# Performance work log

Measured on AMD Instinct MI355X. Metric: run time of the kernel, lower is better.

Reference implementation:

```python
import jax, jax.numpy as jnp
import numpy as np

PATCH = 15  # patch_size (odd, per extract_patches arithmetic)


def _extract_patches(vol, centroids, P):
    """vol: (B,C,H,W,D) float; centroids: (B,N,3) int (x->H, y->W, z->D).
    Returns (B,N,C,P,P,P) with the valid region placed at the patch origin and
    zero padding at the high end of each axis (matches F.pad end-padding)."""
    B, C, H, Wd, D = vol.shape
    half = P // 2
    c = centroids.astype(jnp.int32)                      # (B,N,3)
    dims = jnp.array([H, Wd, D], dtype=jnp.int32)
    starts = jnp.maximum(c - half, 0)                    # (B,N,3)
    ends = jnp.minimum(c + half + 1, dims)               # (B,N,3)
    r = jnp.arange(P, dtype=jnp.int32)
    idx = starts[..., None] + r                          # (B,N,3,P)
    mask = idx < ends[..., None]                         # (B,N,3,P)
    idxc = jnp.minimum(idx, (dims - 1)[None, None, :, None])  # clamp for safe gather

    def one(vol_b, ix, iy, iz, m):
        # vol_b (C,H,W,D); ix/iy/iz (N,P); m (N,3,P)
        p = vol_b[:, ix[:, :, None, None], iy[:, None, :, None], iz[:, None, None, :]]
        p = jnp.transpose(p, (1, 0, 2, 3, 4))            # (N,C,P,P,P)
        m3 = (m[:, 0][:, :, None, None]
              & m[:, 1][:, None, :, None]
              & m[:, 2][:, None, None, :])               # (N,P,P,P)
        return jnp.where(m3[:, None], p, jnp.zeros((), vol_b.dtype))

    return jax.vmap(one)(vol, idxc[:, :, 0], idxc[:, :, 1], idxc[:, :, 2], mask)


def setup_inputs() -> dict:
    key = jax.random.key(0)
    k1, k2, k3 = jax.random.split(key, 3)
    B, C, H, W_, D = 2, 32, 96, 96, 96
    N, F = 64, 1024
    P = PATCH
    x = jax.random.normal(k1, (B, C, H, W_, D), dtype=jnp.float32)
    centroids = jax.random.randint(k2, (B, N, 3), 0, 96, dtype=jnp.int32)
    W = jax.random.normal(k3, (C * P ** 3, F), dtype=jnp.float32) * 0.01
    b = jnp.zeros((F,), dtype=jnp.float32)
    return {"x": x, "centroids": centroids, "W": W, "b": b}


def reference(x, centroids, W, b):
    P = PATCH
    patches = _extract_patches(x, centroids, P)          # (B,N,C,P,P,P)
    B, N = patches.shape[:2]
    flat = patches.reshape(B * N, -1)                    # (B*N, C*P^3)
    out = flat @ W + b                                   # feature_extraction_model
    return out.reshape(B, N, -1)
```

## Files before the change

### kernel.cpp

```cpp
#include <hip/hip_runtime.h>

typedef __attribute__((ext_vector_type(8))) __bf16 bf16x8;
typedef __attribute__((ext_vector_type(8))) unsigned short ushort8;
typedef __attribute__((ext_vector_type(4))) float f32x4;

constexpr int C_ = 32, NN = 64;
constexpr int PK = 3375;
constexpr int K_TOT = 108000;
constexpr int F_TOT = 1024;
constexpr int M_TOT = 128;
constexpr int KSTEPS = 3375;

constexpr int WPAIR  = 2064;
constexpr int WBUF   = 16 * WPAIR;
constexpr int ABUF   = 8192;

__device__ __forceinline__ unsigned short f2bf(float f) {
    unsigned int b = __builtin_bit_cast(unsigned int, f);
    b += 0x7FFFu + ((b >> 16) & 1u);
    return (unsigned short)(b >> 16);
}

__device__ __forceinline__ void async_copy16(void* lds, const void* g) {
    __builtin_amdgcn_global_load_lds(
        (const __attribute__((address_space(1))) unsigned int*)g,
        (__attribute__((address_space(3))) unsigned int*)lds, 16, 0, 0);
}

__global__ void extract_kernel(const float* __restrict__ x,
                               const int* __restrict__ cent,
                               unsigned short* __restrict__ Af) {
    int m = blockIdx.x;
    int c = blockIdx.y;
    int b = m >> 6, n = m & 63;
    int cx = cent[(b * NN + n) * 3 + 0];
    int cy = cent[(b * NN + n) * 3 + 1];
    int cz = cent[(b * NN + n) * 3 + 2];
    int sx = max(cx - 7, 0), ex = min(cx + 8, 96);
    int sy = max(cy - 7, 0), ey = min(cy + 8, 96);
    int sz = max(cz - 7, 0), ez = min(cz + 8, 96);
    const float* xb = x + (size_t)(b * C_ + c) * (96 * 96 * 96);
    unsigned short* Arow = Af + (size_t)m * K_TOT + (size_t)c * PK;
    for (int k = threadIdx.x; k < PK; k += blockDim.x) {
        int iz = k % 15;
        int t  = k / 15;
        int iy = t % 15;
        int ix = t / 15;
        int hx = sx + ix, wy = sy + iy, dz = sz + iz;
        float v = 0.0f;
        if (hx < ex && wy < ey && dz < ez)
            v = xb[(hx * 96 + wy) * 96 + dz];
        Arow[k] = f2bf(v);
    }
}

__global__ __launch_bounds__(256, 1) void gemm_kernel(const unsigned short* __restrict__ Af,
                                                      const float* __restrict__ W,
                                                      float* __restrict__ partial,
                                                      int CS) {
    __shared__ __align__(16) unsigned char smem[2 * WBUF + 2 * ABUF];
    int s  = blockIdx.x;
    int fx = blockIdx.y;
    int st0 = s * CS;
    int st1 = min(st0 + CS, KSTEPS);
    int f0  = fx * 256;

    int tid  = (int)threadIdx.x;
    int wave = tid >> 6, lane = tid & 63;
    int fr = lane & 15, lgrp = lane >> 4;

    f32x4 acc[8][4];
#pragma unroll
    for (int i = 0; i < 8; ++i)
#pragma unroll
        for (int j = 0; j < 4; ++j) acc[i][j] = (f32x4)(0.0f);

    auto STAGE = [&](int buf, int st) {
        int k0 = st << 5;
        unsigned char* wb = smem + buf * WBUF;
        const float* wsrc = W + (size_t)k0 * F_TOT + f0 + (lane << 2);
#pragma unroll
        for (int r = 0; r < 8; ++r) {
            int row = r * 4 + wave;
            async_copy16(wb + (row >> 1) * WPAIR + (row & 1) * 1024,
                         wsrc + (size_t)row * F_TOT);
        }
        unsigned char* ab = smem + 2 * WBUF + buf * ABUF;
        const unsigned short* ag = Af + (size_t)fr * K_TOT + k0 + lgrp * 8;
#pragma unroll
        for (int i = 0; i < 2; ++i) {
            int mt = wave * 2 + i;
            async_copy16(ab + mt * 1024, ag + (size_t)(mt * 16) * K_TOT);
        }
    };

    auto COMPUTE = [&](int buf) {
        const unsigned char* ab = smem + 2 * WBUF + buf * ABUF;
        const unsigned char* wb = smem + buf * WBUF;
        bf16x8 afrag[8];
#pragma unroll
        for (int mt = 0; mt < 8; ++mt)
            afrag[mt] = *reinterpret_cast<const bf16x8*>(ab + mt * 1024 + lane * 16);
#pragma unroll
        for (int ft = 0; ft < 4; ++ft) {
            int fl4 = (wave * 64 + ft * 16 + fr) * 4;
            float wv[8];
#pragma unroll
            for (int j = 0; j < 8; ++j) {
                int row = lgrp * 8 + j;
                wv[j] = *reinterpret_cast<const float*>(
                            wb + (row >> 1) * WPAIR + (row & 1) * 1024 + fl4);
            }
            ushort8 bt;
#pragma unroll
            for (int j = 0; j < 8; ++j) bt[j] = f2bf(wv[j]);
            bf16x8 bfrag = __builtin_bit_cast(bf16x8, bt);
#pragma unroll
            for (int mt = 0; mt < 8; ++mt)
                acc[mt][ft] = __builtin_amdgcn_mfma_f32_16x16x32_bf16(afrag[mt], bfrag, acc[mt][ft], 0, 0, 0);
        }
    };

    int cur = 0;
    STAGE(0, st0);
    for (int t = st0; t < st1 - 1; ++t) {
        STAGE(cur ^ 1, t + 1);
        asm volatile("s_waitcnt vmcnt(10)" ::: "memory");
        __builtin_amdgcn_s_barrier();
        COMPUTE(cur);
        __builtin_amdgcn_s_barrier();
        cur ^= 1;
    }
    asm volatile("s_waitcnt vmcnt(0)" ::: "memory");
    __builtin_amdgcn_s_barrier();
    COMPUTE(cur);

    float* pout = partial + (size_t)s * (M_TOT * F_TOT);
#pragma unroll
    for (int mt = 0; mt < 8; ++mt) {
        int mbase = mt * 16 + lgrp * 4;
#pragma unroll
        for (int ft = 0; ft < 4; ++ft) {
            int f = f0 + wave * 64 + ft * 16 + fr;
#pragma unroll
            for (int r = 0; r < 4; ++r)
                pout[(size_t)(mbase + r) * F_TOT + f] = acc[mt][ft][r];
        }
    }
}

__global__ void reduce_kernel(const float* __restrict__ partial,
                              const float* __restrict__ bias,
                              float* __restrict__ out, int S) {
    int i4 = (blockIdx.x * blockDim.x + threadIdx.x) * 4;
    if (i4 >= M_TOT * F_TOT) return;
    f32x4 a = *reinterpret_cast<const f32x4*>(bias + (i4 & (F_TOT - 1)));
    for (int s = 0; s < S; ++s)
        a += *reinterpret_cast<const f32x4*>(partial + (size_t)s * (M_TOT * F_TOT) + i4);
    *reinterpret_cast<f32x4*>(out + i4) = a;
}

extern "C" void kernel_launch(void* const* d_in, const int* in_sizes, int n_in,
                              void* d_out, int out_size, void* d_ws, size_t ws_size,
                              hipStream_t stream) {
    const float* x    = (const float*)d_in[0];
    const int*   cent = (const int*)d_in[1];
    const float* W    = (const float*)d_in[2];
    const float* bias = (const float*)d_in[3];
    float* out = (float*)d_out;

    unsigned short* Af = (unsigned short*)d_ws;
    size_t Af_bytes = (size_t)M_TOT * K_TOT * 2;
    float* partial = (float*)((char*)d_ws + Af_bytes);

    size_t avail = ws_size > Af_bytes ? ws_size - Af_bytes : 0;
    int S = (int)(avail / ((size_t)M_TOT * F_TOT * 4));
    if (S > 64) S = 64;
    if (S < 1)  S = 1;
    int CS = (KSTEPS + S - 1) / S;
    S = (KSTEPS + CS - 1) / CS;

    extract_kernel<<<dim3(M_TOT, C_), 256, 0, stream>>>(x, cent, Af);
    gemm_kernel<<<dim3(S, 4), 256, 0, stream>>>(Af, W, partial, CS);
    reduce_kernel<<<dim3((M_TOT * F_TOT + 1023) / 1024, 1, 1), 256, 0, stream>>>(partial, bias, out, S);
}
```

Before: 143.6 us.

## Give each wave a private LDS region and drop block barriers in GEMM

Each wave now stages its own 64-column W slice and the full 128-row A tile into a private 32 KB LDS region, so the loop no longer needs workgroup barriers, only per-wave vmcnt waits. This removes the cross-wave synchronisation stalls. In exchange every wave loads the whole A tile itself, so A traffic is four times higher. LDS use grows to 128 KB, and the W layout loses its bank-conflict padding.

Measured after the change: 167.0 us. 1.16x slower.

```diff
diff --git a/kernel.cpp b/kernel.cpp
--- a/kernel.cpp
+++ b/kernel.cpp
@@ -10,10 +10,6 @@
 constexpr int F_TOT = 1024;
 constexpr int M_TOT = 128;
 constexpr int KSTEPS = 3375;
-
-constexpr int WPAIR  = 2064;
-constexpr int WBUF   = 16 * WPAIR;
-constexpr int ABUF   = 8192;
 
 __device__ __forceinline__ unsigned short f2bf(float f) {
     unsigned int b = __builtin_bit_cast(unsigned int, f);
@@ -58,7 +54,7 @@
                                                       const float* __restrict__ W,
                                                       float* __restrict__ partial,
                                                       int CS) {
-    __shared__ __align__(16) unsigned char smem[2 * WBUF + 2 * ABUF];
+    __shared__ __align__(16) unsigned char smem[4 * 32768];
     int s  = blockIdx.x;
     int fx = blockIdx.y;
     int st0 = s * CS;
@@ -68,6 +64,9 @@
     int tid  = (int)threadIdx.x;
     int wave = tid >> 6, lane = tid & 63;
     int fr = lane & 15, lgrp = lane >> 4;
+    int f0w = f0 + wave * 64;
+
+    unsigned char* region = smem + wave * 32768;
 
     f32x4 acc[8][4];
 #pragma unroll
@@ -77,40 +76,32 @@
 
     auto STAGE = [&](int buf, int st) {
         int k0 = st << 5;
-        unsigned char* wb = smem + buf * WBUF;
-        const float* wsrc = W + (size_t)k0 * F_TOT + f0 + (lane << 2);
+        unsigned char* wb = region + buf * 16384;
+        const float* wsrc = W + ((size_t)k0 + (lane >> 4)) * F_TOT + f0w + ((lane & 15) << 2);
 #pragma unroll
-        for (int r = 0; r < 8; ++r) {
-            int row = r * 4 + wave;
-            async_copy16(wb + (row >> 1) * WPAIR + (row & 1) * 1024,
-                         wsrc + (size_t)row * F_TOT);
-        }
-        unsigned char* ab = smem + 2 * WBUF + buf * ABUF;
+        for (int r = 0; r < 8; ++r)
+            async_copy16(wb + r * 1024, wsrc + (size_t)(r * 4) * F_TOT);
+        unsigned char* ab = wb + 8192;
         const unsigned short* ag = Af + (size_t)fr * K_TOT + k0 + lgrp * 8;
 #pragma unroll
-        for (int i = 0; i < 2; ++i) {
-            int mt = wave * 2 + i;
+        for (int mt = 0; mt < 8; ++mt)
             async_copy16(ab + mt * 1024, ag + (size_t)(mt * 16) * K_TOT);
-        }
     };
 
     auto COMPUTE = [&](int buf) {
-        const unsigned char* ab = smem + 2 * WBUF + buf * ABUF;
-        const unsigned char* wb = smem + buf * WBUF;
+        const unsigned char* wb = region + buf * 16384;
+        const unsigned char* ab = wb + 8192;
         bf16x8 afrag[8];
 #pragma unroll
         for (int mt = 0; mt < 8; ++mt)
             afrag[mt] = *reinterpret_cast<const bf16x8*>(ab + mt * 1024 + lane * 16);
 #pragma unroll
         for (int ft = 0; ft < 4; ++ft) {
-            int fl4 = (wave * 64 + ft * 16 + fr) * 4;
+            int fl4 = (ft * 16 + fr) << 2;
             float wv[8];
 #pragma unroll
-            for (int j = 0; j < 8; ++j) {
-                int row = lgrp * 8 + j;
-                wv[j] = *reinterpret_cast<const float*>(
-                            wb + (row >> 1) * WPAIR + (row & 1) * 1024 + fl4);
-            }
+            for (int j = 0; j < 8; ++j)
+                wv[j] = *reinterpret_cast<const float*>(wb + (lgrp * 8 + j) * 256 + fl4);
             ushort8 bt;
 #pragma unroll
             for (int j = 0; j < 8; ++j) bt[j] = f2bf(wv[j]);
@@ -125,14 +116,11 @@
     STAGE(0, st0);
     for (int t = st0; t < st1 - 1; ++t) {
         STAGE(cur ^ 1, t + 1);
-        asm volatile("s_waitcnt vmcnt(10)" ::: "memory");
-        __builtin_amdgcn_s_barrier();
+        asm volatile("s_waitcnt vmcnt(16)" ::: "memory");
         COMPUTE(cur);
-        __builtin_amdgcn_s_barrier();
         cur ^= 1;
     }
     asm volatile("s_waitcnt vmcnt(0)" ::: "memory");
-    __builtin_amdgcn_s_barrier();
     COMPUTE(cur);
 
     float* pout = partial + (size_t)s * (M_TOT * F_TOT);
@@ -141,7 +129,7 @@
         int mbase = mt * 16 + lgrp * 4;
 #pragma unroll
         for (int ft = 0; ft < 4; ++ft) {
-            int f = f0 + wave * 64 + ft * 16 + fr;
+            int f = f0w + ft * 16 + fr;
 #pragma unroll
             for (int r = 0; r < 4; ++r)
                 pout[(size_t)(mbase + r) * F_TOT + f] = acc[mt][ft][r];
```

## Triple-buffer GEMM staging and store split-K partials in bf16

Applied to the files above, without the earlier changes.

The GEMM main loop moves from double to triple buffering, so two K-steps of W and A tiles are in flight while one is computed, with waitcnt thresholds adjusted to match. Split-K partial sums are now written as bf16 instead of fp32, halving partial-buffer traffic, and the reduce kernel reads 8 bf16 values per thread and accumulates in fp32. The bf16 partials lose precision in the reduction, and the larger LDS footprint raises shared-memory use per block.

Measured after the change: 141.0 us. No clear change (-1.8%).

```diff
diff --git a/kernel.cpp b/kernel.cpp
--- a/kernel.cpp
+++ b/kernel.cpp
@@ -14,6 +14,7 @@
 constexpr int WPAIR  = 2064;
 constexpr int WBUF   = 16 * WPAIR;
 constexpr int ABUF   = 8192;
+constexpr int RBUF   = WBUF + ABUF;
 
 __device__ __forceinline__ unsigned short f2bf(float f) {
     unsigned int b = __builtin_bit_cast(unsigned int, f);
@@ -56,9 +57,9 @@
 
 __global__ __launch_bounds__(256, 1) void gemm_kernel(const unsigned short* __restrict__ Af,
                                                       const float* __restrict__ W,
-                                                      float* __restrict__ partial,
+                                                      unsigned short* __restrict__ partial,
                                                       int CS) {
-    __shared__ __align__(16) unsigned char smem[2 * WBUF + 2 * ABUF];
+    __shared__ __align__(16) unsigned char smem[3 * RBUF];
     int s  = blockIdx.x;
     int fx = blockIdx.y;
     int st0 = s * CS;
@@ -77,7 +78,7 @@
 
     auto STAGE = [&](int buf, int st) {
         int k0 = st << 5;
-        unsigned char* wb = smem + buf * WBUF;
+        unsigned char* wb = smem + buf * RBUF;
         const float* wsrc = W + (size_t)k0 * F_TOT + f0 + (lane << 2);
 #pragma unroll
         for (int r = 0; r < 8; ++r) {
@@ -85,7 +86,7 @@
             async_copy16(wb + (row >> 1) * WPAIR + (row & 1) * 1024,
                          wsrc + (size_t)row * F_TOT);
         }
-        unsigned char* ab = smem + 2 * WBUF + buf * ABUF;
+        unsigned char* ab = wb + WBUF;
         const unsigned short* ag = Af + (size_t)fr * K_TOT + k0 + lgrp * 8;
 #pragma unroll
         for (int i = 0; i < 2; ++i) {
@@ -95,8 +96,8 @@
     };
 
     auto COMPUTE = [&](int buf) {
-        const unsigned char* ab = smem + 2 * WBUF + buf * ABUF;
-        const unsigned char* wb = smem + buf * WBUF;
+        const unsigned char* wb = smem + buf * RBUF;
+        const unsigned char* ab = wb + WBUF;
         bf16x8 afrag[8];
 #pragma unroll
         for (int mt = 0; mt < 8; ++mt)
@@ -121,21 +122,32 @@
         }
     };
 
-    int cur = 0;
+    int len = st1 - st0;
     STAGE(0, st0);
-    for (int t = st0; t < st1 - 1; ++t) {
-        STAGE(cur ^ 1, t + 1);
+    if (len > 1) STAGE(1, st0 + 1);
+    int t = st0, cb = 0;
+    for (; t + 2 < st1; ++t) {
+        int sb = cb + 2; if (sb >= 3) sb -= 3;
+        STAGE(sb, t + 2);
+        asm volatile("s_waitcnt vmcnt(20)" ::: "memory");
+        __builtin_amdgcn_s_barrier();
+        COMPUTE(cb);
+        __builtin_amdgcn_s_barrier();
+        if (++cb == 3) cb = 0;
+    }
+    if (t + 1 < st1) {
         asm volatile("s_waitcnt vmcnt(10)" ::: "memory");
         __builtin_amdgcn_s_barrier();
-        COMPUTE(cur);
-        __builtin_amdgcn_s_barrier();
-        cur ^= 1;
+        COMPUTE(cb);
+        __builtin_amdgcn_s_barrier();
+        if (++cb == 3) cb = 0;
+        ++t;
     }
     asm volatile("s_waitcnt vmcnt(0)" ::: "memory");
     __builtin_amdgcn_s_barrier();
-    COMPUTE(cur);
-
-    float* pout = partial + (size_t)s * (M_TOT * F_TOT);
+    COMPUTE(cb);
+
+    unsigned short* pout = partial + (size_t)s * (M_TOT * F_TOT);
 #pragma unroll
     for (int mt = 0; mt < 8; ++mt) {
         int mbase = mt * 16 + lgrp * 4;
@@ -144,20 +156,27 @@
             int f = f0 + wave * 64 + ft * 16 + fr;
 #pragma unroll
             for (int r = 0; r < 4; ++r)
-                pout[(size_t)(mbase + r) * F_TOT + f] = acc[mt][ft][r];
-        }
-    }
-}
-
-__global__ void reduce_kernel(const float* __restrict__ partial,
+                pout[(size_t)(mbase + r) * F_TOT + f] = f2bf(acc[mt][ft][r]);
+        }
+    }
+}
+
+__global__ void reduce_kernel(const unsigned short* __restrict__ partial,
                               const float* __restrict__ bias,
                               float* __restrict__ out, int S) {
-    int i4 = (blockIdx.x * blockDim.x + threadIdx.x) * 4;
-    if (i4 >= M_TOT * F_TOT) return;
-    f32x4 a = *reinterpret_cast<const f32x4*>(bias + (i4 & (F_TOT - 1)));
-    for (int s = 0; s < S; ++s)
-        a += *reinterpret_cast<const f32x4*>(partial + (size_t)s * (M_TOT * F_TOT) + i4);
-    *reinterpret_cast<f32x4*>(out + i4) = a;
+    int i8 = (blockIdx.x * blockDim.x + threadIdx.x) * 8;
+    if (i8 >= M_TOT * F_TOT) return;
+    float a[8];
+#pragma unroll
+    for (int j = 0; j < 8; ++j) a[j] = bias[(i8 & (F_TOT - 1)) + j];
+    for (int s = 0; s < S; ++s) {
+        ushort8 p = *reinterpret_cast<const ushort8*>(partial + (size_t)s * (M_TOT * F_TOT) + i8);
+#pragma unroll
+        for (int j = 0; j < 8; ++j)
+            a[j] += __builtin_bit_cast(float, (unsigned int)p[j] << 16);
+    }
+#pragma unroll
+    for (int j = 0; j < 8; ++j) out[i8 + j] = a[j];
 }
 
 extern "C" void kernel_launch(void* const* d_in, const int* in_sizes, int n_in,
@@ -171,10 +190,10 @@
 
     unsigned short* Af = (unsigned short*)d_ws;
     size_t Af_bytes = (size_t)M_TOT * K_TOT * 2;
-    float* partial = (float*)((char*)d_ws + Af_bytes);
+    unsigned short* partial = (unsigned short*)((char*)d_ws + Af_bytes);
 
     size_t avail = ws_size > Af_bytes ? ws_size - Af_bytes : 0;
-    int S = (int)(avail / ((size_t)M_TOT * F_TOT * 4));
+    int S = (int)(avail / ((size_t)M_TOT * F_TOT * 2));
     if (S > 64) S = 64;
     if (S < 1)  S = 1;
     int CS = (KSTEPS + S - 1) / S;
@@ -182,5 +201,5 @@
 
     extract_kernel<<<dim3(M_TOT, C_), 256, 0, stream>>>(x, cent, Af);
     gemm_kernel<<<dim3(S, 4), 256, 0, stream>>>(Af, W, partial, CS);
-    reduce_kernel<<<dim3((M_TOT * F_TOT + 1023) / 1024, 1, 1), 256, 0, stream>>>(partial, bias, out, S);
-}
+    reduce_kernel<<<dim3((M_TOT * F_TOT) / (256 * 8)), 256, 0, stream>>>(partial, bias, out, S);
+}
```
